# Optimization experiments

Hardware: AMD Instinct MI355X
Metric: run time of the kernel (lower is better)

The kernel has to match this reference:

```python
import jax, jax.numpy as jnp
import numpy as np


def _perm_mats():
    E = np.zeros((36, 9), np.float32)
    D = np.zeros((9, 36), np.float32)
    c = 0
    for i in range(8):
        for j in range(i + 1, 9):
            E[c, i] = 1.0
            E[c, j] = 1.0
            D[i, c] = 1.0
            D[j, c] = 1.0
            c += 1
    assert c == 36
    return E, D


def setup_inputs() -> dict:
    key = jax.random.key(0)
    B = 32768
    # binary candidate mask: [B, 9 digits, 9 rows, 9 cols]
    mask = jnp.round(jax.random.uniform(key, (B, 9, 9, 9), dtype=jnp.float32))
    E, D = _perm_mats()
    return {"mask": mask, "enc": jnp.asarray(E), "dec": jnp.asarray(D)}


def _nn_compare(x, v):
    # NNCompare: triangular bump == 1 exactly when x == v (for integer-valued x)
    return jnp.minimum(jax.nn.relu(x - (v - 1.0)), jax.nn.relu((v + 1.0) - x))


def _nn_and(x, y):
    return jnp.clip(jnp.minimum(x, y), 0.0, 1.0)


def reference(mask, enc, dec):
    B = mask.shape[0]
    # encode_permutations: 1x1 conv 9 -> 36 (pair selection)
    perms = jnp.einsum('oc,bchw->bohw', enc, mask)          # [B,36,9,9]
    perms = _nn_compare(perms, 2.0)                          # cell contains exactly this pair
    # sum_all_permutations: 1x1 conv 36 -> 1, then == 1
    sum_p = _nn_compare(jnp.sum(perms, axis=1, keepdims=True), 1.0)  # [B,1,9,9]
    perms = _nn_and(perms, sum_p)                            # broadcast over 36 channels
    # box downsample: grouped 3x3 stride-3 sum conv
    down = perms.reshape(B, 36, 3, 3, 3, 3).sum(axis=(3, 5))  # [B,36,3,3]
    down = _nn_compare(down, 2.0)                              # exactly two such cells in box
    up = jnp.repeat(jnp.repeat(down, 3, axis=2), 3, axis=3)    # [B,36,9,9]
    up = _nn_and(up, 1.0 - perms)                              # other cells in the box
    # decode_permutations: 1x1 conv 36 -> 9
    erase = jnp.einsum('oc,bchw->bohw', dec, up)               # [B,9,9,9]
    return _nn_and(mask, 1.0 - erase)
```

## Files before the change

kernel.cpp:

```cpp
#include <hip/hip_runtime.h>
#include <stdint.h>


#define NB 8
#define ELEMS (NB * 729)
#define NWORDS (ELEMS / 4)
#define NCELL (NB * 81)

__global__ __launch_bounds__(256) void sudoku_naked_pair_kernel(
    const float* __restrict__ mask, float* __restrict__ out) {
  __shared__ uint32_t bits32[NWORDS];
  __shared__ unsigned short cellm[NCELL];
  __shared__ unsigned short pairm[NCELL];
  uint8_t* bits = (uint8_t*)bits32;

  const int tid = threadIdx.x;
  const size_t base = (size_t)blockIdx.x * ELEMS;

  const float4* in4 = (const float4*)(mask + base);
  for (int i = tid; i < NWORDS; i += 256) {
    float4 v = in4[i];
    uint32_t w = (uint32_t)(v.x != 0.0f)
               | ((uint32_t)(v.y != 0.0f) << 8)
               | ((uint32_t)(v.z != 0.0f) << 16)
               | ((uint32_t)(v.w != 0.0f) << 24);
    bits32[i] = w;
  }
  __syncthreads();

  for (int c = tid; c < NCELL; c += 256) {
    int b = c / 81, cell = c - b * 81;
    const uint8_t* p = bits + b * 729 + cell;
    uint32_t m = 0;
#pragma unroll
    for (int d = 0; d < 9; ++d) m |= ((uint32_t)p[d * 81] & 1u) << d;
    cellm[c] = (unsigned short)m;
    pairm[c] = (__popc(m) == 2) ? (unsigned short)m : 0;
  }
  __syncthreads();

  for (int c = tid; c < NCELL; c += 256) {
    int b = c / 81, cell = c - b * 81;
    int r = cell / 9, col = cell - r * 9;
    int bb = b * 81 + (r / 3) * 27 + (col / 3) * 3;
    uint32_t pm[9];
#pragma unroll
    for (int j = 0; j < 3; ++j) {
      pm[3 * j + 0] = pairm[bb + 9 * j + 0];
      pm[3 * j + 1] = pairm[bb + 9 * j + 1];
      pm[3 * j + 2] = pairm[bb + 9 * j + 2];
    }
    uint32_t mypair = pairm[c];
    uint32_t er = 0;
#pragma unroll
    for (int j = 0; j < 9; ++j) {
      uint32_t p = pm[j];
      int cnt = 0;
#pragma unroll
      for (int k = 0; k < 9; ++k) cnt += (pm[k] == p);
      if (p && cnt == 2 && p != mypair) er |= p;
    }
    uint32_t fin = (uint32_t)cellm[c] & ~er;
    cellm[c] = (unsigned short)fin;
  }
  __syncthreads();

  float4* out4 = (float4*)(out + base);
  for (int i = tid; i < NWORDS; i += 256) {
    int e0 = i * 4;
    float4 v;
    float* vp = &v.x;
#pragma unroll
    for (int q = 0; q < 4; ++q) {
      int e = e0 + q;
      int b = e / 729;
      int rem = e - b * 729;
      int d = rem / 81;
      int cell = rem - d * 81;
      vp[q] = (float)((cellm[b * 81 + cell] >> d) & 1u);
    }
    out4[i] = v;
  }
}

extern "C" void kernel_launch(void* const* d_in, const int* in_sizes, int n_in,
                              void* d_out, int out_size, void* d_ws, size_t ws_size,
                              hipStream_t stream) {
  const float* mask = (const float*)d_in[0];
  float* out = (float*)d_out;
  int B = in_sizes[0] / 729;
  int grid = B / NB;
  sudoku_naked_pair_kernel<<<grid, 256, 0, stream>>>(mask, out);
}
```

Baseline: 178.6 us.

## Load cell masks directly from global, compute per-box erase masks, drop byte staging

Each thread now reads its cell's nine digit planes straight from global memory with scalar strided loads and keeps the 9-bit mask in registers, instead of staging a byte copy of the whole block in shared memory. Naked-pair detection is done once per box by 72 threads, which write per-cell erase masks to shared memory. Output is written as scalar strided stores per cell. This removes a shared-memory pass and a barrier and dedupes the box work, but swaps float4 vector loads and stores for scalar ones. Because lanes hold consecutive cells, accesses should still coalesce within a digit plane.

After: 174.6 us. 2.2% less time.

```diff
diff --git a/kernel.cpp b/kernel.cpp
--- a/kernel.cpp
+++ b/kernel.cpp
@@ -3,46 +3,38 @@
 
 
 #define NB 8
-#define ELEMS (NB * 729)
-#define NWORDS (ELEMS / 4)
 #define NCELL (NB * 81)
+#define NBOX (NB * 9)
+#define CPT 3
 
 __global__ __launch_bounds__(256) void sudoku_naked_pair_kernel(
     const float* __restrict__ mask, float* __restrict__ out) {
-  __shared__ uint32_t bits32[NWORDS];
-  __shared__ unsigned short cellm[NCELL];
   __shared__ unsigned short pairm[NCELL];
-  uint8_t* bits = (uint8_t*)bits32;
+  __shared__ unsigned short erls[NCELL];
 
   const int tid = threadIdx.x;
-  const size_t base = (size_t)blockIdx.x * ELEMS;
+  const size_t base = (size_t)blockIdx.x * (NB * 729);
 
-  const float4* in4 = (const float4*)(mask + base);
-  for (int i = tid; i < NWORDS; i += 256) {
-    float4 v = in4[i];
-    uint32_t w = (uint32_t)(v.x != 0.0f)
-               | ((uint32_t)(v.y != 0.0f) << 8)
-               | ((uint32_t)(v.z != 0.0f) << 16)
-               | ((uint32_t)(v.w != 0.0f) << 24);
-    bits32[i] = w;
+  uint32_t mycell[CPT];
+
+#pragma unroll
+  for (int it = 0; it < CPT; ++it) {
+    const int c = tid + it * 256;
+    if (c < NCELL) {
+      const int b = c / 81, cell = c - b * 81;
+      const float* p = mask + base + b * 729 + cell;
+      uint32_t m = 0;
+#pragma unroll
+      for (int d = 0; d < 9; ++d) m |= (p[d * 81] != 0.0f ? 1u : 0u) << d;
+      mycell[it] = m;
+      pairm[c] = (unsigned short)((__popc(m) == 2) ? m : 0u);
+    }
   }
   __syncthreads();
 
-  for (int c = tid; c < NCELL; c += 256) {
-    int b = c / 81, cell = c - b * 81;
-    const uint8_t* p = bits + b * 729 + cell;
-    uint32_t m = 0;
-#pragma unroll
-    for (int d = 0; d < 9; ++d) m |= ((uint32_t)p[d * 81] & 1u) << d;
-    cellm[c] = (unsigned short)m;
-    pairm[c] = (__popc(m) == 2) ? (unsigned short)m : 0;
-  }
-  __syncthreads();
-
-  for (int c = tid; c < NCELL; c += 256) {
-    int b = c / 81, cell = c - b * 81;
-    int r = cell / 9, col = cell - r * 9;
-    int bb = b * 81 + (r / 3) * 27 + (col / 3) * 3;
+  if (tid < NBOX) {
+    const int b = tid / 9, bi = tid - b * 9;
+    const int bb = b * 81 + (bi / 3) * 27 + (bi % 3) * 3;
     uint32_t pm[9];
 #pragma unroll
     for (int j = 0; j < 3; ++j) {
@@ -50,36 +42,36 @@
       pm[3 * j + 1] = pairm[bb + 9 * j + 1];
       pm[3 * j + 2] = pairm[bb + 9 * j + 2];
     }
-    uint32_t mypair = pairm[c];
-    uint32_t er = 0;
+    bool naked[9];
 #pragma unroll
     for (int j = 0; j < 9; ++j) {
-      uint32_t p = pm[j];
       int cnt = 0;
 #pragma unroll
-      for (int k = 0; k < 9; ++k) cnt += (pm[k] == p);
-      if (p && cnt == 2 && p != mypair) er |= p;
+      for (int k = 0; k < 9; ++k) cnt += (pm[k] == pm[j]);
+      naked[j] = (pm[j] != 0u) && (cnt == 2);
     }
-    uint32_t fin = (uint32_t)cellm[c] & ~er;
-    cellm[c] = (unsigned short)fin;
+#pragma unroll
+    for (int j = 0; j < 9; ++j) {
+      uint32_t er = 0;
+#pragma unroll
+      for (int k = 0; k < 9; ++k)
+        if (naked[k] && pm[k] != pm[j]) er |= pm[k];
+      const int cell = bb + 9 * (j / 3) + (j % 3);
+      erls[cell] = (unsigned short)er;
+    }
   }
   __syncthreads();
 
-  float4* out4 = (float4*)(out + base);
-  for (int i = tid; i < NWORDS; i += 256) {
-    int e0 = i * 4;
-    float4 v;
-    float* vp = &v.x;
 #pragma unroll
-    for (int q = 0; q < 4; ++q) {
-      int e = e0 + q;
-      int b = e / 729;
-      int rem = e - b * 729;
-      int d = rem / 81;
-      int cell = rem - d * 81;
-      vp[q] = (float)((cellm[b * 81 + cell] >> d) & 1u);
+  for (int it = 0; it < CPT; ++it) {
+    const int c = tid + it * 256;
+    if (c < NCELL) {
+      const int b = c / 81, cell = c - b * 81;
+      const uint32_t fin = mycell[it] & ~(uint32_t)erls[c];
+      float* q = out + base + b * 729 + cell;
+#pragma unroll
+      for (int d = 0; d < 9; ++d) q[d * 81] = (float)((fin >> d) & 1u);
     }
-    out4[i] = v;
   }
 }
 
@@ -88,7 +80,7 @@
                               hipStream_t stream) {
   const float* mask = (const float*)d_in[0];
   float* out = (float*)d_out;
-  int B = in_sizes[0] / 729;
-  int grid = B / NB;
+  const int B = in_sizes[0] / 729;
+  const int grid = B / NB;
   sudoku_naked_pair_kernel<<<grid, 256, 0, stream>>>(mask, out);
 }
```
